# Kernel tuning notes

Hardware: AMD Instinct MI355X
Metric: run time of the kernel (lower is better)

The kernel has to match this reference:

```python
import jax, jax.numpy as jnp
import numpy as np

S_LEN, BATCH, HID, HEADS = 2048, 4, 1024, 16
HD = HID // HEADS


def setup_inputs() -> dict:
    key = jax.random.key(0)
    ks = jax.random.split(key, 6)

    def lin_w(k, out_dim, in_dim):
        return jax.random.normal(k, (out_dim, in_dim), jnp.float32) * (1.0 / np.sqrt(in_dim))

    return {
        "hidden_states": jax.random.normal(ks[0], (S_LEN, BATCH, HID), jnp.float32),
        "Wq": lin_w(ks[1], HID, HID), "bq": jnp.zeros((HID,), jnp.float32),
        "Wk": lin_w(ks[2], HID, HID), "bk": jnp.zeros((HID,), jnp.float32),
        "Wv": lin_w(ks[3], HID, HID), "bv": jnp.zeros((HID,), jnp.float32),
        "Wf": lin_w(ks[4], HEADS, HID), "bf": jnp.zeros((HEADS,), jnp.float32),
        "Wo": lin_w(ks[5], HID, HID), "bo": jnp.zeros((HID,), jnp.float32),
    }


def _forget_attention(hidden_states, Wq, bq, Wk, bk, Wv, bv, Wf, bf, Wo, bo):
    S, B, H = hidden_states.shape
    nh, hd = HEADS, HD

    def shape(x):
        return x.reshape(S, B, nh, hd)

    q = shape(hidden_states @ Wq.T + bq)
    k = shape(hidden_states @ Wk.T + bk)
    v = shape(hidden_states @ Wv.T + bv)

    # kernel_fn = elu(x) + 1
    phi_q = jax.nn.elu(q) + 1.0
    phi_k = jax.nn.elu(k) + 1.0

    f = jax.nn.sigmoid(hidden_states @ Wf.T + bf)  # [S, B, nh]

    # F_{t,j} = prod_{i=j+1}^{t} f_i  factorizes into the recurrence:
    #   S_t = f_t * S_{t-1} + phi_k_t (x) v_t ;  z_t = f_t * z_{t-1} + phi_k_t
    # out_t = (phi_q_t . S_t) / (phi_q_t . z_t + eps)
    def step(carry, xs):
        Sm, z = carry                      # [B,nh,hd,hd], [B,nh,hd]
        ft, pk, pq, vt = xs                # [B,nh], [B,nh,hd] x3
        fte = ft[..., None]
        Sm = fte[..., None] * Sm + pk[..., :, None] * vt[..., None, :]
        z = fte * z + pk
        num = jnp.einsum('bhd,bhde->bhe', pq, Sm)
        den = jnp.einsum('bhd,bhd->bh', pq, z)[..., None]
        return (Sm, z), num / (den + 1e-6)

    init = (jnp.zeros((B, nh, hd, hd), hidden_states.dtype),
            jnp.zeros((B, nh, hd), hidden_states.dtype))
    _, out = jax.lax.scan(step, init, (f, phi_k, phi_q, v))

    out = out.reshape(S, B, H) @ Wo.T + bo
    return out, f


def reference(hidden_states, Wq, bq, Wk, bk, Wv, bv, Wf, bf, Wo, bo):
    out, f = _forget_attention(hidden_states, Wq, bq, Wk, bk, Wv, bv, Wf, bf, Wo, bo)
    return (out, jnp.zeros_like(out), f)
```

## Files before the change

### kernel.cpp

```cpp
#include <hip/hip_runtime.h>
#include <hip/hip_bf16.h>
#include <math.h>

#define S_LEN 2048
#define BATCH 4
#define HID   1024
#define HEADS 16
#define HD    64
#define SB    (S_LEN*BATCH)
#define CHUNK 64
#define NCHUNK (S_LEN/CHUNK)
#define BH    (BATCH*HEADS)
#define NSTK  3200

typedef __bf16 bf16x8 __attribute__((ext_vector_type(8)));
typedef float  f32x4  __attribute__((ext_vector_type(4)));
typedef unsigned short ushort_t;
typedef unsigned short u16x8 __attribute__((ext_vector_type(8)));

__device__ __forceinline__ unsigned short f2bf(float x) {
    union { float f; unsigned int u; } un; un.f = x;
    unsigned int u = un.u;
    unsigned int r = (u + 0x7FFFu + ((u >> 16) & 1u)) >> 16;
    return (unsigned short)r;
}
__device__ __forceinline__ float bf2f(unsigned short s) {
    union { unsigned int u; float f; } un; un.u = ((unsigned int)s) << 16;
    return un.f;
}

#define NXU (SB*HID/4)
#define NW1 (NSTK*HID/4)
#define NW2 (HID*HID/4)
#define NBU (NSTK/4)
#define NTOT (NXU+NW1+NW2+NBU)

__global__ __launch_bounds__(256) void prep_kernel(
    const float* __restrict__ X,  const float* __restrict__ Wq,
    const float* __restrict__ Wk, const float* __restrict__ Wv,
    const float* __restrict__ Wf, const float* __restrict__ Wo,
    const float* __restrict__ bq, const float* __restrict__ bk,
    const float* __restrict__ bv, const float* __restrict__ bf,
    ushort_t* __restrict__ Xb, ushort_t* __restrict__ Wstk,
    ushort_t* __restrict__ Wob, float* __restrict__ bstk)
{
    const int i = blockIdx.x * 256 + threadIdx.x;
    if (i < NXU) {
        float4 v = ((const float4*)X)[i];
        ushort4 o; o.x=f2bf(v.x); o.y=f2bf(v.y); o.z=f2bf(v.z); o.w=f2bf(v.w);
        ((ushort4*)Xb)[i] = o;
    } else if (i < NXU + NW1) {
        const int idx4 = (i - NXU) * 4;
        const int row = idx4 >> 10, col = idx4 & 1023;
        float4 v;
        if      (row < 1024) v = *(const float4*)(Wq + (size_t)row*HID + col);
        else if (row < 2048) v = *(const float4*)(Wk + (size_t)(row-1024)*HID + col);
        else if (row < 3072) v = *(const float4*)(Wv + (size_t)(row-2048)*HID + col);
        else if (row < 3088) v = *(const float4*)(Wf + (size_t)(row-3072)*HID + col);
        else                 v = make_float4(0.f,0.f,0.f,0.f);
        ushort4 o; o.x=f2bf(v.x); o.y=f2bf(v.y); o.z=f2bf(v.z); o.w=f2bf(v.w);
        *(ushort4*)(Wstk + idx4) = o;
    } else if (i < NXU + NW1 + NW2) {
        const int idx4 = (i - NXU - NW1) * 4;
        float4 v = *(const float4*)(Wo + idx4);
        ushort4 o; o.x=f2bf(v.x); o.y=f2bf(v.y); o.z=f2bf(v.z); o.w=f2bf(v.w);
        *(ushort4*)(Wob + idx4) = o;
    } else if (i < NTOT) {
        const int idx4 = (i - NXU - NW1 - NW2) * 4;
        #pragma unroll
        for (int t = 0; t < 4; ++t) {
            const int c = idx4 + t;
            float v;
            if      (c < 1024) v = bq[c];
            else if (c < 2048) v = bk[c-1024];
            else if (c < 3072) v = bv[c-2048];
            else if (c < 3088) v = bf[c-3072];
            else               v = 0.f;
            bstk[c] = v;
        }
    }
}

__global__ __launch_bounds__(256) void qkvf_gemm(
    const ushort_t* __restrict__ X, const ushort_t* __restrict__ W,
    const float* __restrict__ bias,
    ushort_t* __restrict__ Q, ushort_t* __restrict__ Kr,
    ushort_t* __restrict__ V,
    float* __restrict__ f_out, float* __restrict__ logf_out)
{
    __shared__ ushort_t As[128 * 32];
    __shared__ ushort_t Bs[128 * 32];

    const int tid  = threadIdx.x;
    const int wave = tid >> 6, lane = tid & 63;
    const int waveM = wave >> 1, waveN = wave & 1;
    const int rowBase = blockIdx.x * 128;
    const int colBase = blockIdx.y * 128;
    const int K = HID;

    f32x4 acc[4][4];
    #pragma unroll
    for (int i = 0; i < 4; ++i)
        #pragma unroll
        for (int j = 0; j < 4; ++j)
            acc[i][j] = (f32x4){0.f, 0.f, 0.f, 0.f};

    const int srow = lane >> 2;
    const int scol = (lane & 3) * 8;

    const ushort_t* gA0 = X + (size_t)(rowBase + wave*16 + srow) * K + scol;
    const ushort_t* gB0 = W + (size_t)(colBase + wave*16 + srow) * K + scol;
    ushort_t* lA = As + (wave*16)*32;
    ushort_t* lB = Bs + (wave*16)*32;

    const int fr = lane & 15;
    const int fk = (lane >> 4) * 8;

    for (int k0 = 0; k0 < K; k0 += 32) {
        __builtin_amdgcn_global_load_lds(
            (const __attribute__((address_space(1))) void*)(gA0 + k0),
            (__attribute__((address_space(3))) void*)lA, 16, 0, 0);
        __builtin_amdgcn_global_load_lds(
            (const __attribute__((address_space(1))) void*)(gA0 + (size_t)64*K + k0),
            (__attribute__((address_space(3))) void*)(lA + 64*32), 16, 0, 0);
        __builtin_amdgcn_global_load_lds(
            (const __attribute__((address_space(1))) void*)(gB0 + k0),
            (__attribute__((address_space(3))) void*)lB, 16, 0, 0);
        __builtin_amdgcn_global_load_lds(
            (const __attribute__((address_space(1))) void*)(gB0 + (size_t)64*K + k0),
            (__attribute__((address_space(3))) void*)(lB + 64*32), 16, 0, 0);

        __syncthreads();

        bf16x8 a[4], b[4];
        #pragma unroll
        for (int i = 0; i < 4; ++i)
            a[i] = *(const bf16x8*)(As + (waveM*64 + i*16 + fr)*32 + fk);
        #pragma unroll
        for (int j = 0; j < 4; ++j)
            b[j] = *(const bf16x8*)(Bs + (waveN*64 + j*16 + fr)*32 + fk);

        #pragma unroll
        for (int i = 0; i < 4; ++i)
            #pragma unroll
            for (int j = 0; j < 4; ++j)
                acc[i][j] = __builtin_amdgcn_mfma_f32_16x16x32_bf16(
                    a[i], b[j], acc[i][j], 0, 0, 0);

        __syncthreads();
    }

    const int er = (lane >> 4) * 4;
    const int ec = lane & 15;
    #pragma unroll
    for (int i = 0; i < 4; ++i) {
        #pragma unroll
        for (int j = 0; j < 4; ++j) {
            const int r0 = rowBase + waveM*64 + i*16 + er;
            const int c0 = colBase + waveN*64 + j*16;
            if (c0 >= 3088) continue;
            const int c  = c0 + ec;
            const float bv = bias[c];
            #pragma unroll
            for (int k = 0; k < 4; ++k) {
                float v = acc[i][j][k] + bv;
                const int r = r0 + k;
                if (c0 < 1024) {
                    v = (v > 0.f) ? (v + 1.f) : __expf(v);
                    Q[(size_t)r * HID + c] = f2bf(v);
                } else if (c0 < 2048) {
                    v = (v > 0.f) ? (v + 1.f) : __expf(v);
                    Kr[(size_t)r * HID + (c - 1024)] = f2bf(v);
                } else if (c0 < 3072) {
                    V[(size_t)r * HID + (c - 2048)] = f2bf(v);
                } else {
                    const int n = c - 3072;
                    const float fv = 1.f / (1.f + __expf(-v));
                    f_out[(size_t)r * HEADS + n]    = fv;
                    logf_out[(size_t)r * HEADS + n] = -__logf(1.f + __expf(-v));
                }
            }
        }
    }
}

__global__ __launch_bounds__(256) void gemm_out(
    const ushort_t* __restrict__ X, const ushort_t* __restrict__ W,
    const float* __restrict__ bias, float* __restrict__ Y,
    float* __restrict__ Yzero)
{
    __shared__ ushort_t As[128 * 32];
    __shared__ ushort_t Bs[128 * 32];

    const int tid  = threadIdx.x;
    const int wave = tid >> 6, lane = tid & 63;
    const int waveM = wave >> 1, waveN = wave & 1;
    const int rowBase = blockIdx.x * 128;
    const int colBase = blockIdx.y * 128;
    const int K = HID, N = HID;

    f32x4 acc[4][4];
    #pragma unroll
    for (int i = 0; i < 4; ++i)
        #pragma unroll
        for (int j = 0; j < 4; ++j)
            acc[i][j] = (f32x4){0.f, 0.f, 0.f, 0.f};

    const int srow = lane >> 2;
    const int scol = (lane & 3) * 8;

    const ushort_t* gA0 = X + (size_t)(rowBase + wave*16 + srow) * K + scol;
    const ushort_t* gB0 = W + (size_t)(colBase + wave*16 + srow) * K + scol;
    ushort_t* lA = As + (wave*16)*32;
    ushort_t* lB = Bs + (wave*16)*32;

    const int fr = lane & 15;
    const int fk = (lane >> 4) * 8;

    for (int k0 = 0; k0 < K; k0 += 32) {
        __builtin_amdgcn_global_load_lds(
            (const __attribute__((address_space(1))) void*)(gA0 + k0),
            (__attribute__((address_space(3))) void*)lA, 16, 0, 0);
        __builtin_amdgcn_global_load_lds(
            (const __attribute__((address_space(1))) void*)(gA0 + (size_t)64*K + k0),
            (__attribute__((address_space(3))) void*)(lA + 64*32), 16, 0, 0);
        __builtin_amdgcn_global_load_lds(
            (const __attribute__((address_space(1))) void*)(gB0 + k0),
            (__attribute__((address_space(3))) void*)lB, 16, 0, 0);
        __builtin_amdgcn_global_load_lds(
            (const __attribute__((address_space(1))) void*)(gB0 + (size_t)64*K + k0),
            (__attribute__((address_space(3))) void*)(lB + 64*32), 16, 0, 0);

        __syncthreads();

        bf16x8 a[4], b[4];
        #pragma unroll
        for (int i = 0; i < 4; ++i)
            a[i] = *(const bf16x8*)(As + (waveM*64 + i*16 + fr)*32 + fk);
        #pragma unroll
        for (int j = 0; j < 4; ++j)
            b[j] = *(const bf16x8*)(Bs + (waveN*64 + j*16 + fr)*32 + fk);

        #pragma unroll
        for (int i = 0; i < 4; ++i)
            #pragma unroll
            for (int j = 0; j < 4; ++j)
                acc[i][j] = __builtin_amdgcn_mfma_f32_16x16x32_bf16(
                    a[i], b[j], acc[i][j], 0, 0, 0);

        __syncthreads();
    }

    const int er = (lane >> 4) * 4;
    const int ec = lane & 15;
    #pragma unroll
    for (int i = 0; i < 4; ++i) {
        #pragma unroll
        for (int j = 0; j < 4; ++j) {
            const int r0 = rowBase + waveM*64 + i*16 + er;
            const int c  = colBase + waveN*64 + j*16 + ec;
            const float bv = bias[c];
            #pragma unroll
            for (int k = 0; k < 4; ++k) {
                const size_t off = (size_t)(r0 + k) * N + c;
                Y[off] = acc[i][j][k] + bv;
                Yzero[off] = 0.f;
            }
        }
    }
}

__global__ __launch_bounds__(256) void pass1_kernel(
    const ushort_t* __restrict__ Kp, const ushort_t* __restrict__ Vp,
    const float* __restrict__ logf,
    ushort_t* __restrict__ Schunk, float* __restrict__ zchunk,
    float* __restrict__ Dchunk)
{
    __shared__ __align__(16) char smem[18688];
    ushort_t* vsT = (ushort_t*)smem;
    ushort_t* kTd = (ushort_t*)(smem + 9216);
    float*    exd = (float*)(smem + 18432);

    const int chunk = blockIdx.x;
    const int bh = blockIdx.y;
    const int b = bh >> 4, h = bh & 15;
    const int tid = threadIdx.x;
    const int wv = tid >> 6, ln = tid & 63;
    const int fr = ln & 15, q4 = ln >> 4;
    const size_t slot = (size_t)bh * NCHUNK + chunk;

    u16x8 vreg[2], kreg[2];
    #pragma unroll
    for (int it = 0; it < 2; ++it) {
        const int u = it*256 + tid;
        const int j = u >> 3, d8 = (u & 7) * 8;
        const size_t base = (size_t)((chunk*64 + j)*BATCH + b)*HID + h*HD + d8;
        vreg[it] = *(const u16x8*)(Vp + base);
        kreg[it] = *(const u16x8*)(Kp + base);
    }
    if (tid < 64) {
        float v = logf[(size_t)((chunk*64 + tid)*BATCH + b) * HEADS + h];
        #pragma unroll
        for (int off = 1; off < 64; off <<= 1) {
            float n = __shfl_up(v, off);
            if (tid >= off) v += n;
        }
        const float tot = __shfl(v, 63);
        exd[tid] = __expf(tot - v);
        if (tid == 63) Dchunk[slot] = __expf(tot);
    }
    __syncthreads();

    #pragma unroll
    for (int it = 0; it < 2; ++it) {
        const int u = it*256 + tid;
        const int j = u >> 3, d8 = (u & 7) * 8;
        const float ex = exd[j];
        #pragma unroll
        for (int i = 0; i < 8; ++i) {
            vsT[(d8+i)*72 + j] = vreg[it][i];
            kTd[(d8+i)*72 + j] = f2bf(bf2f(kreg[it][i]) * ex);
        }
    }
    __syncthreads();

    f32x4 acc[4];
    #pragma unroll
    for (int nt = 0; nt < 4; ++nt) acc[nt] = (f32x4){0.f,0.f,0.f,0.f};
    #pragma unroll
    for (int k0 = 0; k0 < 64; k0 += 32) {
        bf16x8 av = *(const bf16x8*)(vsT + (wv*16 + fr)*72 + k0 + q4*8);
        #pragma unroll
        for (int nt = 0; nt < 4; ++nt) {
            bf16x8 bk = *(const bf16x8*)(kTd + (nt*16 + fr)*72 + k0 + q4*8);
            acc[nt] = __builtin_amdgcn_mfma_f32_16x16x32_bf16(av, bk, acc[nt], 0, 0, 0);
        }
    }

    if (wv == 0) {
        u16x8 onesu;
        #pragma unroll
        for (int i = 0; i < 8; ++i) onesu[i] = 0x3F80;
        const bf16x8 ones = *(const bf16x8*)&onesu;
        f32x4 zacc[4];
        #pragma unroll
        for (int nt = 0; nt < 4; ++nt) zacc[nt] = (f32x4){0.f,0.f,0.f,0.f};
        #pragma unroll
        for (int k0 = 0; k0 < 64; k0 += 32) {
            #pragma unroll
            for (int nt = 0; nt < 4; ++nt) {
                bf16x8 bk = *(const bf16x8*)(kTd + (nt*16 + fr)*72 + k0 + q4*8);
                zacc[nt] = __builtin_amdgcn_mfma_f32_16x16x32_bf16(ones, bk, zacc[nt], 0, 0, 0);
            }
        }
        if (q4 == 0) {
            #pragma unroll
            for (int nt = 0; nt < 4; ++nt)
                zchunk[slot*64 + nt*16 + fr] = zacc[nt][0];
        }
    }

    ushort_t* sp = Schunk + slot * 4096;
    #pragma unroll
    for (int nt = 0; nt < 4; ++nt) {
        #pragma unroll
        for (int r = 0; r < 4; ++r) {
            const int e = wv*16 + q4*4 + r;
            sp[e*64 + nt*16 + fr] = f2bf(acc[nt][r]);
        }
    }
}

__global__ __launch_bounds__(256) void pass2_kernel(
    ushort_t* __restrict__ Schunk, float* __restrict__ zchunk,
    const float* __restrict__ Dchunk)
{
    const int bh = blockIdx.x;
    const int tid = threadIdx.x;

    float Sprev[16];
    #pragma unroll
    for (int i = 0; i < 16; ++i) Sprev[i] = 0.f;
    float zprev = 0.f;

    const size_t base  = (size_t)bh * NCHUNK * 4096;
    const size_t zbase = (size_t)bh * NCHUNK * 64;

    ushort_t b0[16], b1[16];
    float z0v = 0.f, z1v = 0.f;
    #pragma unroll
    for (int i = 0; i < 16; ++i) {
        b0[i] = Schunk[base + 0*4096 + i*256 + tid];
        b1[i] = Schunk[base + 1*4096 + i*256 + tid];
    }
    if (tid < 64) {
        z0v = zchunk[zbase + 0*64 + tid];
        z1v = zchunk[zbase + 1*64 + tid];
    }

    for (int c = 0; c < NCHUNK; ++c) {
        const float D = Dchunk[bh * NCHUNK + c];
        ushort_t* sp = Schunk + base + (size_t)c * 4096;
        #pragma unroll
        for (int i = 0; i < 16; ++i) {
            const float contrib = bf2f(b0[i]);
            sp[i*256 + tid] = f2bf(Sprev[i]);
            Sprev[i] = D * Sprev[i] + contrib;
            b0[i] = b1[i];
        }
        if (tid < 64) {
            const float zc = z0v;
            zchunk[zbase + (size_t)c * 64 + tid] = zprev;
            zprev = D * zprev + zc;
            z0v = z1v;
        }
        if (c + 2 < NCHUNK) {
            #pragma unroll
            for (int i = 0; i < 16; ++i)
                b1[i] = Schunk[base + (size_t)(c+2)*4096 + i*256 + tid];
            if (tid < 64) z1v = zchunk[zbase + (size_t)(c+2)*64 + tid];
        }
    }
}

__global__ __launch_bounds__(256) void pass3_kernel(
    const ushort_t* __restrict__ Qp, const ushort_t* __restrict__ Kp,
    const ushort_t* __restrict__ Vp, const float* __restrict__ logf,
    const ushort_t* __restrict__ S0, const float* __restrict__ z0,
    ushort_t* __restrict__ AO)
{
    __shared__ __align__(16) char smem[28928];
    ushort_t* qs  = (ushort_t*)smem;
    ushort_t* ks  = (ushort_t*)(smem + 9216);
    ushort_t* vsT = (ushort_t*)(smem + 9216);
    ushort_t* psA = (ushort_t*)(smem + 18432);
    float* cc  = (float*)(smem + 27648);
    float* exT = (float*)(smem + 27904);
    float* qz  = (float*)(smem + 28160);
    float* den = (float*)(smem + 28416);
    float* zz  = (float*)(smem + 28672);

    const int chunk = blockIdx.x;
    const int bh = blockIdx.y;
    const int b = bh >> 4, h = bh & 15;
    const int tid = threadIdx.x;
    const int wv = tid >> 6, ln = tid & 63;
    const int fr = ln & 15, q4 = ln >> 4;
    const size_t slot = (size_t)bh * NCHUNK + chunk;

    u16x8 vreg[2];
    #pragma unroll
    for (int it = 0; it < 2; ++it) {
        const int u = it*256 + tid;
        const int j = u >> 3, d8 = (u & 7) * 8;
        vreg[it] = *(const u16x8*)(Vp + (size_t)((chunk*64 + j)*BATCH + b)*HID + h*HD + d8);
    }

    if (tid < 64) {
        zz[tid] = z0[slot * 64 + tid];
        float v = logf[(size_t)((chunk*64 + tid)*BATCH + b) * HEADS + h];
        #pragma unroll
        for (int off = 1; off < 64; off <<= 1) {
            float n = __shfl_up(v, off);
            if (tid >= off) v += n;
        }
        cc[tid]  = v;
        exT[tid] = __expf(v);
    }
    #pragma unroll
    for (int it = 0; it < 2; ++it) {
        const int u = it*256 + tid;
        const int r = u >> 3, c8 = (u & 7) * 8;
        const size_t goff = (size_t)((chunk*64 + r)*BATCH + b) * HID + h*HD + c8;
        *(u16x8*)(qs + r*72 + c8) = *(const u16x8*)(Qp + goff);
        *(u16x8*)(ks + r*72 + c8) = *(const u16x8*)(Kp + goff);
    }
    __syncthreads();

    f32x4 pacc[4];
    #pragma unroll
    for (int nt = 0; nt < 4; ++nt) pacc[nt] = (f32x4){0.f,0.f,0.f,0.f};
    #pragma unroll
    for (int k0 = 0; k0 < 64; k0 += 32) {
        bf16x8 af = *(const bf16x8*)(qs + (wv*16 + fr)*72 + k0 + q4*8);
        #pragma unroll
        for (int nt = 0; nt < 4; ++nt) {
            bf16x8 bfr = *(const bf16x8*)(ks + (nt*16 + fr)*72 + k0 + q4*8);
            pacc[nt] = __builtin_amdgcn_mfma_f32_16x16x32_bf16(af, bfr, pacc[nt], 0, 0, 0);
        }
    }
    {
        const int t = wv*16 + fr;
        const int d0 = q4 * 16;
        float s = 0.f;
        #pragma unroll
        for (int i = 0; i < 16; ++i)
            s += bf2f(qs[t*72 + d0 + i]) * zz[d0 + i];
        s += __shfl_xor(s, 16);
        s += __shfl_xor(s, 32);
        if (q4 == 0) qz[t] = s;
    }
    __syncthreads();

    #pragma unroll
    for (int it = 0; it < 2; ++it) {
        const int u = it*256 + tid;
        const int j = u >> 3, d8 = (u & 7) * 8;
        #pragma unroll
        for (int i = 0; i < 8; ++i)
            vsT[(d8+i)*72 + j] = vreg[it][i];
    }
    {
        float rs[4] = {0.f, 0.f, 0.f, 0.f};
        float cct[4];
        #pragma unroll
        for (int r = 0; r < 4; ++r) cct[r] = cc[wv*16 + q4*4 + r];
        #pragma unroll
        for (int nt = 0; nt < 4; ++nt) {
            const int j = nt*16 + fr;
            const float ccj = cc[j];
            #pragma unroll
            for (int r = 0; r < 4; ++r) {
                const int t = wv*16 + q4*4 + r;
                float p = (j <= t) ? pacc[nt][r] * __expf(cct[r] - ccj) : 0.f;
                rs[r] += p;
                psA[t*72 + j] = f2bf(p);
            }
        }
        #pragma unroll
        for (int m = 1; m < 16; m <<= 1) {
            #pragma unroll
            for (int r = 0; r < 4; ++r) rs[r] += __shfl_xor(rs[r], m);
        }
        if (fr == 0) {
            #pragma unroll
            for (int r = 0; r < 4; ++r) {
                const int t = wv*16 + q4*4 + r;
                den[t] = rs[r] + exT[t] * qz[t] + 1e-6f;
            }
        }
    }
    __syncthreads();

    f32x4 oacc[4], oacc2[4];
    #pragma unroll
    for (int nt = 0; nt < 4; ++nt) {
        oacc[nt]  = (f32x4){0.f,0.f,0.f,0.f};
        oacc2[nt] = (f32x4){0.f,0.f,0.f,0.f};
    }
    const ushort_t* S0p = S0 + slot * 4096;
    #pragma unroll
    for (int k0 = 0; k0 < 64; k0 += 32) {
        const int k8 = k0 + q4*8;
        bf16x8 ap = *(const bf16x8*)(psA + (wv*16 + fr)*72 + k8);
        bf16x8 aq = *(const bf16x8*)(qs  + (wv*16 + fr)*72 + k8);
        #pragma unroll
        for (int nt = 0; nt < 4; ++nt) {
            bf16x8 bv = *(const bf16x8*)(vsT + (nt*16 + fr)*72 + k8);
            oacc[nt] = __builtin_amdgcn_mfma_f32_16x16x32_bf16(ap, bv, oacc[nt], 0, 0, 0);
            bf16x8 sb = *(const bf16x8*)(S0p + (nt*16 + fr)*64 + k8);
            oacc2[nt] = __builtin_amdgcn_mfma_f32_16x16x32_bf16(aq, sb, oacc2[nt], 0, 0, 0);
        }
    }
    #pragma unroll
    for (int nt = 0; nt < 4; ++nt) {
        const int e = nt*16 + fr;
        #pragma unroll
        for (int r = 0; r < 4; ++r) {
            const int t = wv*16 + q4*4 + r;
            const float v = (oacc[nt][r] + exT[t] * oacc2[nt][r]) / den[t];
            AO[(size_t)((chunk*64 + t)*BATCH + b) * HID + h*HD + e] = f2bf(v);
        }
    }
}

extern "C" void kernel_launch(void* const* d_in, const int* in_sizes, int n_in,
                              void* d_out, int out_size, void* d_ws, size_t ws_size,
                              hipStream_t stream) {
    const float* X  = (const float*)d_in[0];
    const float* Wq = (const float*)d_in[1];
    const float* bq = (const float*)d_in[2];
    const float* Wk = (const float*)d_in[3];
    const float* bk = (const float*)d_in[4];
    const float* Wv = (const float*)d_in[5];
    const float* bv = (const float*)d_in[6];
    const float* Wf = (const float*)d_in[7];
    const float* bf = (const float*)d_in[8];
    const float* Wo = (const float*)d_in[9];
    const float* bo = (const float*)d_in[10];

    float* out = (float*)d_out;
    const size_t OUT_SLOT = (size_t)SB * HID;

    char* ws = (char*)d_ws;
    ushort_t* wsXb   = (ushort_t*)ws;
    ushort_t* wsWstk = wsXb + (size_t)SB * HID;
    ushort_t* wsWob  = wsWstk + (size_t)NSTK * HID;
    ushort_t* wsQ    = wsWob + (size_t)HID * HID;
    ushort_t* wsK    = wsQ + (size_t)SB * HID;
    ushort_t* wsV    = wsK + (size_t)SB * HID;
    float* wsBstk = (float*)(wsV + (size_t)SB * HID);
    float* wsLogf = wsBstk + NSTK;
    ushort_t* wsS  = (ushort_t*)(wsLogf + (size_t)SB * HEADS);
    float* wsZ    = (float*)(wsS + (size_t)BH * NCHUNK * HD * HD);
    float* wsD    = wsZ + (size_t)BH * NCHUNK * HD;

    prep_kernel<<<(NTOT + 255)/256, 256, 0, stream>>>(
        X, Wq, Wk, Wv, Wf, Wo, bq, bk, bv, bf,
        wsXb, wsWstk, wsWob, wsBstk);

    dim3 qgrid(SB/128, NSTK/128);
    qkvf_gemm<<<qgrid, 256, 0, stream>>>(
        wsXb, wsWstk, wsBstk, wsQ, wsK, wsV,
        out + 2*OUT_SLOT, wsLogf);

    dim3 sgrid(NCHUNK, BH);
    pass1_kernel<<<sgrid, 256, 0, stream>>>(wsK, wsV, wsLogf, wsS, wsZ, wsD);
    pass2_kernel<<<BH, 256, 0, stream>>>(wsS, wsZ, wsD);
    pass3_kernel<<<sgrid, 256, 0, stream>>>(wsQ, wsK, wsV, wsLogf, wsS, wsZ, wsXb);

    dim3 ogrid(SB/128, HID/128);
    gemm_out<<<ogrid, 256, 0, stream>>>(wsXb, wsWob, bo, out, out + OUT_SLOT);
}
```

Baseline: 290.5 us.

## Double-buffer LDS in both GEMMs, memset zero output, cache chunk decays in LDS

```diff
diff --git a/kernel.cpp b/kernel.cpp
--- a/kernel.cpp
+++ b/kernel.cpp
@@ -28,6 +28,10 @@
     union { unsigned int u; float f; } un; un.u = ((unsigned int)s) << 16;
     return un.f;
 }
+
+#define GLL16(src, dst) __builtin_amdgcn_global_load_lds( \
+    (const __attribute__((address_space(1))) void*)(src), \
+    (__attribute__((address_space(3))) void*)(dst), 16, 0, 0)
 
 #define NXU (SB*HID/4)
 #define NW1 (NSTK*HID/4)
@@ -88,8 +92,8 @@
     ushort_t* __restrict__ V,
     float* __restrict__ f_out, float* __restrict__ logf_out)
 {
-    __shared__ ushort_t As[128 * 32];
-    __shared__ ushort_t Bs[128 * 32];
+    __shared__ ushort_t As[2][128 * 32];
+    __shared__ ushort_t Bs[2][128 * 32];
 
     const int tid  = threadIdx.x;
     const int wave = tid >> 6, lane = tid & 63;
@@ -110,35 +114,41 @@
 
     const ushort_t* gA0 = X + (size_t)(rowBase + wave*16 + srow) * K + scol;
     const ushort_t* gB0 = W + (size_t)(colBase + wave*16 + srow) * K + scol;
-    ushort_t* lA = As + (wave*16)*32;
-    ushort_t* lB = Bs + (wave*16)*32;
+    const int ldsWaveOff = (wave*16)*32;
 
     const int fr = lane & 15;
     const int fk = (lane >> 4) * 8;
 
+    {
+        ushort_t* lA = As[0] + ldsWaveOff;
+        ushort_t* lB = Bs[0] + ldsWaveOff;
+        GLL16(gA0,                  lA);
+        GLL16(gA0 + (size_t)64*K,   lA + 64*32);
+        GLL16(gB0,                  lB);
+        GLL16(gB0 + (size_t)64*K,   lB + 64*32);
+    }
+    __syncthreads();
+
+    int cur = 0;
+    #pragma unroll 2
     for (int k0 = 0; k0 < K; k0 += 32) {
-        __builtin_amdgcn_global_load_lds(
-            (const __attribute__((address_space(1))) void*)(gA0 + k0),
-            (__attribute__((address_space(3))) void*)lA, 16, 0, 0);
-        __builtin_amdgcn_global_load_lds(
-            (const __attribute__((address_space(1))) void*)(gA0 + (size_t)64*K + k0),
-            (__attribute__((address_space(3))) void*)(lA + 64*32), 16, 0, 0);
-        __builtin_amdgcn_global_load_lds(
-            (const __attribute__((address_space(1))) void*)(gB0 + k0),
-            (__attribute__((address_space(3))) void*)lB, 16, 0, 0);
-        __builtin_amdgcn_global_load_lds(
-            (const __attribute__((address_space(1))) void*)(gB0 + (size_t)64*K + k0),
-            (__attribute__((address_space(3))) void*)(lB + 64*32), 16, 0, 0);
-
-        __syncthreads();
+        if (k0 + 32 < K) {
+            const int nxt = cur ^ 1;
+            ushort_t* lA = As[nxt] + ldsWaveOff;
+            ushort_t* lB = Bs[nxt] + ldsWaveOff;
+            GLL16(gA0 + k0 + 32,                lA);
+            GLL16(gA0 + (size_t)64*K + k0 + 32, lA + 64*32);
+            GLL16(gB0 + k0 + 32,                lB);
+            GLL16(gB0 + (size_t)64*K + k0 + 32, lB + 64*32);
+        }
 
         bf16x8 a[4], b[4];
         #pragma unroll
         for (int i = 0; i < 4; ++i)
-            a[i] = *(const bf16x8*)(As + (waveM*64 + i*16 + fr)*32 + fk);
+            a[i] = *(const bf16x8*)(As[cur] + (waveM*64 + i*16 + fr)*32 + fk);
         #pragma unroll
         for (int j = 0; j < 4; ++j)
-            b[j] = *(const bf16x8*)(Bs + (waveN*64 + j*16 + fr)*32 + fk);
+            b[j] = *(const bf16x8*)(Bs[cur] + (waveN*64 + j*16 + fr)*32 + fk);
 
         #pragma unroll
         for (int i = 0; i < 4; ++i)
@@ -148,6 +158,7 @@
                     a[i], b[j], acc[i][j], 0, 0, 0);
 
         __syncthreads();
+        cur ^= 1;
     }
 
     const int er = (lane >> 4) * 4;
@@ -186,11 +197,10 @@
 
 __global__ __launch_bounds__(256) void gemm_out(
     const ushort_t* __restrict__ X, const ushort_t* __restrict__ W,
-    const float* __restrict__ bias, float* __restrict__ Y,
-    float* __restrict__ Yzero)
+    const float* __restrict__ bias, float* __restrict__ Y)
 {
-    __shared__ ushort_t As[128 * 32];
-    __shared__ ushort_t Bs[128 * 32];
+    __shared__ ushort_t As[2][128 * 32];
+    __shared__ ushort_t Bs[2][128 * 32];
 
     const int tid  = threadIdx.x;
     const int wave = tid >> 6, lane = tid & 63;
@@ -211,35 +221,41 @@
 
     const ushort_t* gA0 = X + (size_t)(rowBase + wave*16 + srow) * K + scol;
     const ushort_t* gB0 = W + (size_t)(colBase + wave*16 + srow) * K + scol;
-    ushort_t* lA = As + (wave*16)*32;
-    ushort_t* lB = Bs + (wave*16)*32;
+    const int ldsWaveOff = (wave*16)*32;
 
     const int fr = lane & 15;
     const int fk = (lane >> 4) * 8;
 
+    {
+        ushort_t* lA = As[0] + ldsWaveOff;
+        ushort_t* lB = Bs[0] + ldsWaveOff;
+        GLL16(gA0,                  lA);
+        GLL16(gA0 + (size_t)64*K,   lA + 64*32);
+        GLL16(gB0,                  lB);
+        GLL16(gB0 + (size_t)64*K,   lB + 64*32);
+    }
+    __syncthreads();
+
+    int cur = 0;
+    #pragma unroll 2
     for (int k0 = 0; k0 < K; k0 += 32) {
-        __builtin_amdgcn_global_load_lds(
-            (const __attribute__((address_space(1))) void*)(gA0 + k0),
-            (__attribute__((address_space(3))) void*)lA, 16, 0, 0);
-        __builtin_amdgcn_global_load_lds(
-            (const __attribute__((address_space(1))) void*)(gA0 + (size_t)64*K + k0),
-            (__attribute__((address_space(3))) void*)(lA + 64*32), 16, 0, 0);
-        __builtin_amdgcn_global_load_lds(
-            (const __attribute__((address_space(1))) void*)(gB0 + k0),
-            (__attribute__((address_space(3))) void*)lB, 16, 0, 0);
-        __builtin_amdgcn_global_load_lds(
-            (const __attribute__((address_space(1))) void*)(gB0 + (size_t)64*K + k0),
-            (__attribute__((address_space(3))) void*)(lB + 64*32), 16, 0, 0);
-
-        __syncthreads();
+        if (k0 + 32 < K) {
+            const int nxt = cur ^ 1;
+            ushort_t* lA = As[nxt] + ldsWaveOff;
+            ushort_t* lB = Bs[nxt] + ldsWaveOff;
+            GLL16(gA0 + k0 + 32,                lA);
+            GLL16(gA0 + (size_t)64*K + k0 + 32, lA + 64*32);
+            GLL16(gB0 + k0 + 32,                lB);
+            GLL16(gB0 + (size_t)64*K + k0 + 32, lB + 64*32);
+        }
 
         bf16x8 a[4], b[4];
         #pragma unroll
         for (int i = 0; i < 4; ++i)
-            a[i] = *(const bf16x8*)(As + (waveM*64 + i*16 + fr)*32 + fk);
+            a[i] = *(const bf16x8*)(As[cur] + (waveM*64 + i*16 + fr)*32 + fk);
         #pragma unroll
         for (int j = 0; j < 4; ++j)
-            b[j] = *(const bf16x8*)(Bs + (waveN*64 + j*16 + fr)*32 + fk);
+            b[j] = *(const bf16x8*)(Bs[cur] + (waveN*64 + j*16 + fr)*32 + fk);
 
         #pragma unroll
         for (int i = 0; i < 4; ++i)
@@ -249,6 +265,7 @@
                     a[i], b[j], acc[i][j], 0, 0, 0);
 
         __syncthreads();
+        cur ^= 1;
     }
 
     const int er = (lane >> 4) * 4;
@@ -264,7 +281,6 @@
             for (int k = 0; k < 4; ++k) {
                 const size_t off = (size_t)(r0 + k) * N + c;
                 Y[off] = acc[i][j][k] + bv;
-                Yzero[off] = 0.f;
             }
         }
     }
@@ -375,8 +391,11 @@
     ushort_t* __restrict__ Schunk, float* __restrict__ zchunk,
     const float* __restrict__ Dchunk)
 {
+    __shared__ float Ds[NCHUNK];
     const int bh = blockIdx.x;
     const int tid = threadIdx.x;
+
+    if (tid < NCHUNK) Ds[tid] = Dchunk[bh * NCHUNK + tid];
 
     float Sprev[16];
     #pragma unroll
@@ -397,9 +416,10 @@
         z0v = zchunk[zbase + 0*64 + tid];
         z1v = zchunk[zbase + 1*64 + tid];
     }
+    __syncthreads();
 
     for (int c = 0; c < NCHUNK; ++c) {
-        const float D = Dchunk[bh * NCHUNK + c];
+        const float D = Ds[c];
         ushort_t* sp = Schunk + base + (size_t)c * 4096;
         #pragma unroll
         for (int i = 0; i < 16; ++i) {
@@ -605,6 +625,8 @@
     float* wsZ    = (float*)(wsS + (size_t)BH * NCHUNK * HD * HD);
     float* wsD    = wsZ + (size_t)BH * NCHUNK * HD;
 
+    hipMemsetAsync(out + OUT_SLOT, 0, OUT_SLOT * sizeof(float), stream);
+
     prep_kernel<<<(NTOT + 255)/256, 256, 0, stream>>>(
         X, Wq, Wk, Wv, Wf, Wo, bq, bk, bv, bf,
         wsXb, wsWstk, wsWob, wsBstk);
@@ -620,5 +642,5 @@
     pass3_kernel<<<sgrid, 256, 0, stream>>>(wsQ, wsK, wsV, wsLogf, wsS, wsZ, wsXb);
 
     dim3 ogrid(SB/128, HID/128);
-    gemm_out<<<ogrid, 256, 0, stream>>>(wsXb, wsWob, bo, out, out + OUT_SLOT);
-}
+    gemm_out<<<ogrid, 256, 0, stream>>>(wsXb, wsWob, bo, out);
+}
```

New measurement: 303.1 us. 1.04x slower.

## Rewrite QKVF GEMM with 256x256 tiles and triple-buffered async LDS pipeline

Applied to the files above, without the earlier changes.

```diff
diff --git a/kernel.cpp b/kernel.cpp
--- a/kernel.cpp
+++ b/kernel.cpp
@@ -11,7 +11,7 @@
 #define CHUNK 64
 #define NCHUNK (S_LEN/CHUNK)
 #define BH    (BATCH*HEADS)
-#define NSTK  3200
+#define NSTK  3328
 
 typedef __bf16 bf16x8 __attribute__((ext_vector_type(8)));
 typedef float  f32x4  __attribute__((ext_vector_type(4)));
@@ -28,6 +28,12 @@
     union { unsigned int u; float f; } un; un.u = ((unsigned int)s) << 16;
     return un.f;
 }
+
+#define GLL16(src, dst) __builtin_amdgcn_global_load_lds( \
+    (const __attribute__((address_space(1))) void*)(src), \
+    (__attribute__((address_space(3))) void*)(dst), 16, 0, 0)
+
+#define BAR()  asm volatile("s_barrier" ::: "memory")
 
 #define NXU (SB*HID/4)
 #define NW1 (NSTK*HID/4)
@@ -81,83 +87,121 @@
     }
 }
 
-__global__ __launch_bounds__(256) void qkvf_gemm(
+#define QTILES 32
+#define QBLOCKS 416
+
+__global__ __launch_bounds__(512, 2) void qkvf_gemm256(
     const ushort_t* __restrict__ X, const ushort_t* __restrict__ W,
     const float* __restrict__ bias,
     ushort_t* __restrict__ Q, ushort_t* __restrict__ Kr,
     ushort_t* __restrict__ V,
     float* __restrict__ f_out, float* __restrict__ logf_out)
 {
-    __shared__ ushort_t As[128 * 32];
-    __shared__ ushort_t Bs[128 * 32];
+    __shared__ ushort_t lds[3 * 16384];
 
     const int tid  = threadIdx.x;
     const int wave = tid >> 6, lane = tid & 63;
-    const int waveM = wave >> 1, waveN = wave & 1;
-    const int rowBase = blockIdx.x * 128;
-    const int colBase = blockIdx.y * 128;
+    const int wm = wave >> 2, wn = wave & 3;
+    const int fr = lane & 15, q4 = lane >> 4;
     const int K = HID;
 
-    f32x4 acc[4][4];
-    #pragma unroll
-    for (int i = 0; i < 4; ++i)
+    const int wg = ((blockIdx.x & 7) * 52) + (blockIdx.x >> 3);
+    const int rowBase = (wg & 31) << 8;
+    const int colBase = (wg >> 5) << 8;
+
+    const int sRow = lane >> 2;
+    const int sCol = (((lane & 3) ^ ((lane >> 3) & 3)) << 3);
+    const ushort_t* gA0 = X + (size_t)(rowBase + wave*32 + sRow) * K + sCol;
+    const ushort_t* gB0 = W + (size_t)(colBase + wave*32 + sRow) * K + sCol;
+    const int stA = wave * 1024;
+    const int stB = 8192 + wave * 1024;
+
+    const int sl = ((q4 ^ ((fr >> 1) & 3)) << 3);
+    const int aBase = wm*4096 + fr*32 + sl;
+    const int bBase = 8192 + wn*2048 + fr*32 + sl;
+
+    f32x4 acc[8][4];
+    #pragma unroll
+    for (int i = 0; i < 8; ++i)
         #pragma unroll
         for (int j = 0; j < 4; ++j)
             acc[i][j] = (f32x4){0.f, 0.f, 0.f, 0.f};
 
-    const int srow = lane >> 2;
-    const int scol = (lane & 3) * 8;
-
-    const ushort_t* gA0 = X + (size_t)(rowBase + wave*16 + srow) * K + scol;
-    const ushort_t* gB0 = W + (size_t)(colBase + wave*16 + srow) * K + scol;
-    ushort_t* lA = As + (wave*16)*32;
-    ushort_t* lB = Bs + (wave*16)*32;
-
-    const int fr = lane & 15;
-    const int fk = (lane >> 4) * 8;
-
-    for (int k0 = 0; k0 < K; k0 += 32) {
-        __builtin_amdgcn_global_load_lds(
-            (const __attribute__((address_space(1))) void*)(gA0 + k0),
-            (__attribute__((address_space(3))) void*)lA, 16, 0, 0);
-        __builtin_amdgcn_global_load_lds(
-            (const __attribute__((address_space(1))) void*)(gA0 + (size_t)64*K + k0),
-            (__attribute__((address_space(3))) void*)(lA + 64*32), 16, 0, 0);
-        __builtin_amdgcn_global_load_lds(
-            (const __attribute__((address_space(1))) void*)(gB0 + k0),
-            (__attribute__((address_space(3))) void*)lB, 16, 0, 0);
-        __builtin_amdgcn_global_load_lds(
-            (const __attribute__((address_space(1))) void*)(gB0 + (size_t)64*K + k0),
-            (__attribute__((address_space(3))) void*)(lB + 64*32), 16, 0, 0);
-
-        __syncthreads();
-
-        bf16x8 a[4], b[4];
+    GLL16(gA0,                     lds + stA);
+    GLL16(gA0 + (size_t)16*K,      lds + stA + 512);
+    GLL16(gB0,                     lds + stB);
+    GLL16(gB0 + (size_t)16*K,      lds + stB + 512);
+    GLL16(gA0 + 32,                lds + 16384 + stA);
+    GLL16(gA0 + (size_t)16*K + 32, lds + 16384 + stA + 512);
+    GLL16(gB0 + 32,                lds + 16384 + stB);
+    GLL16(gB0 + (size_t)16*K + 32, lds + 16384 + stB + 512);
+    asm volatile("s_waitcnt vmcnt(4)" ::: "memory");
+    BAR();
+
+    int bi = 0, si = 2;
+    const ushort_t* gAs = gA0 + 64;
+    const ushort_t* gBs = gB0 + 64;
+
+    for (int t = 0; t < QTILES; ++t) {
+        const ushort_t* Lb = lds + bi * 16384;
+        ushort_t* Ls = lds + si * 16384;
+
+        bf16x8 af[4], bfr[4];
         #pragma unroll
         for (int i = 0; i < 4; ++i)
-            a[i] = *(const bf16x8*)(As + (waveM*64 + i*16 + fr)*32 + fk);
+            af[i] = *(const bf16x8*)(Lb + aBase + i*512);
         #pragma unroll
         for (int j = 0; j < 4; ++j)
-            b[j] = *(const bf16x8*)(Bs + (waveN*64 + j*16 + fr)*32 + fk);
-
+            bfr[j] = *(const bf16x8*)(Lb + bBase + j*512);
+        if (t < QTILES - 2) {
+            GLL16(gAs,                Ls + stA);
+            GLL16(gAs + (size_t)16*K, Ls + stA + 512);
+        }
+        BAR();
+        __builtin_amdgcn_s_setprio(1);
         #pragma unroll
         for (int i = 0; i < 4; ++i)
             #pragma unroll
             for (int j = 0; j < 4; ++j)
                 acc[i][j] = __builtin_amdgcn_mfma_f32_16x16x32_bf16(
-                    a[i], b[j], acc[i][j], 0, 0, 0);
-
-        __syncthreads();
-    }
-
-    const int er = (lane >> 4) * 4;
-    const int ec = lane & 15;
-    #pragma unroll
-    for (int i = 0; i < 4; ++i) {
+                    af[i], bfr[j], acc[i][j], 0, 0, 0);
+        __builtin_amdgcn_s_setprio(0);
+        BAR();
+
+        bf16x8 ag[4];
+        #pragma unroll
+        for (int i = 0; i < 4; ++i)
+            ag[i] = *(const bf16x8*)(Lb + aBase + 2048 + i*512);
+        if (t < QTILES - 2) {
+            GLL16(gBs,                Ls + stB);
+            GLL16(gBs + (size_t)16*K, Ls + stB + 512);
+        }
+        BAR();
+        __builtin_amdgcn_s_setprio(1);
+        #pragma unroll
+        for (int i = 0; i < 4; ++i)
+            #pragma unroll
+            for (int j = 0; j < 4; ++j)
+                acc[4+i][j] = __builtin_amdgcn_mfma_f32_16x16x32_bf16(
+                    ag[i], bfr[j], acc[4+i][j], 0, 0, 0);
+        __builtin_amdgcn_s_setprio(0);
+        if (t < QTILES - 2)       { asm volatile("s_waitcnt vmcnt(4)" ::: "memory"); }
+        else if (t == QTILES - 2) { asm volatile("s_waitcnt vmcnt(0)" ::: "memory"); }
+        BAR();
+
+        bi = (bi == 2) ? 0 : bi + 1;
+        si = (si == 2) ? 0 : si + 1;
+        gAs += 32; gBs += 32;
+    }
+
+    const int er = q4 * 4;
+    const int ec = fr;
+    #pragma unroll
+    for (int i = 0; i < 8; ++i) {
         #pragma unroll
         for (int j = 0; j < 4; ++j) {
-            const int r0 = rowBase + waveM*64 + i*16 + er;
-            const int c0 = colBase + waveN*64 + j*16;
+            const int r0 = rowBase + wm*128 + i*16 + er;
+            const int c0 = colBase + wn*64 + j*16;
             if (c0 >= 3088) continue;
             const int c  = c0 + ec;
             const float bv = bias[c];
@@ -186,8 +230,7 @@
 
 __global__ __launch_bounds__(256) void gemm_out(
     const ushort_t* __restrict__ X, const ushort_t* __restrict__ W,
-    const float* __restrict__ bias, float* __restrict__ Y,
-    float* __restrict__ Yzero)
+    const float* __restrict__ bias, float* __restrict__ Y)
 {
     __shared__ ushort_t As[128 * 32];
     __shared__ ushort_t Bs[128 * 32];
@@ -218,18 +261,10 @@
     const int fk = (lane >> 4) * 8;
 
     for (int k0 = 0; k0 < K; k0 += 32) {
-        __builtin_amdgcn_global_load_lds(
-            (const __attribute__((address_space(1))) void*)(gA0 + k0),
-            (__attribute__((address_space(3))) void*)lA, 16, 0, 0);
-        __builtin_amdgcn_global_load_lds(
-            (const __attribute__((address_space(1))) void*)(gA0 + (size_t)64*K + k0),
-            (__attribute__((address_space(3))) void*)(lA + 64*32), 16, 0, 0);
-        __builtin_amdgcn_global_load_lds(
-            (const __attribute__((address_space(1))) void*)(gB0 + k0),
-            (__attribute__((address_space(3))) void*)lB, 16, 0, 0);
-        __builtin_amdgcn_global_load_lds(
-            (const __attribute__((address_space(1))) void*)(gB0 + (size_t)64*K + k0),
-            (__attribute__((address_space(3))) void*)(lB + 64*32), 16, 0, 0);
+        GLL16(gA0 + k0,                lA);
+        GLL16(gA0 + (size_t)64*K + k0, lA + 64*32);
+        GLL16(gB0 + k0,                lB);
+        GLL16(gB0 + (size_t)64*K + k0, lB + 64*32);
 
         __syncthreads();
 
@@ -264,7 +299,6 @@
             for (int k = 0; k < 4; ++k) {
                 const size_t off = (size_t)(r0 + k) * N + c;
                 Y[off] = acc[i][j][k] + bv;
-                Yzero[off] = 0.f;
             }
         }
     }
@@ -375,8 +409,11 @@
     ushort_t* __restrict__ Schunk, float* __restrict__ zchunk,
     const float* __restrict__ Dchunk)
 {
+    __shared__ float Ds[NCHUNK];
     const int bh = blockIdx.x;
     const int tid = threadIdx.x;
+
+    if (tid < NCHUNK) Ds[tid] = Dchunk[bh * NCHUNK + tid];
 
     float Sprev[16];
     #pragma unroll
@@ -397,9 +434,10 @@
         z0v = zchunk[zbase + 0*64 + tid];
         z1v = zchunk[zbase + 1*64 + tid];
     }
+    __syncthreads();
 
     for (int c = 0; c < NCHUNK; ++c) {
-        const float D = Dchunk[bh * NCHUNK + c];
+        const float D = Ds[c];
         ushort_t* sp = Schunk + base + (size_t)c * 4096;
         #pragma unroll
         for (int i = 0; i < 16; ++i) {
@@ -605,12 +643,13 @@
     float* wsZ    = (float*)(wsS + (size_t)BH * NCHUNK * HD * HD);
     float* wsD    = wsZ + (size_t)BH * NCHUNK * HD;
 
+    hipMemsetAsync(out + OUT_SLOT, 0, OUT_SLOT * sizeof(float), stream);
+
     prep_kernel<<<(NTOT + 255)/256, 256, 0, stream>>>(
         X, Wq, Wk, Wv, Wf, Wo, bq, bk, bv, bf,
         wsXb, wsWstk, wsWob, wsBstk);
 
-    dim3 qgrid(SB/128, NSTK/128);
-    qkvf_gemm<<<qgrid, 256, 0, stream>>>(
+    qkvf_gemm256<<<QBLOCKS, 512, 0, stream>>>(
         wsXb, wsWstk, wsBstk, wsQ, wsK, wsV,
         out + 2*OUT_SLOT, wsLogf);
 
@@ -620,5 +659,5 @@
     pass3_kernel<<<sgrid, 256, 0, stream>>>(wsQ, wsK, wsV, wsLogf, wsS, wsZ, wsXb);
 
     dim3 ogrid(SB/128, HID/128);
-    gemm_out<<<ogrid, 256, 0, stream>>>(wsXb, wsWob, bo, out, out + OUT_SLOT);
-}
+    gemm_out<<<ogrid, 256, 0, stream>>>(wsXb, wsWob, bo, out);
+}
```

Result: slower. 362.3 us (+24.8%).

## Split chunk-state scan across 8 blocks per head and memset zero output

Applied to the files above, without the earlier changes.

```diff
diff --git a/kernel.cpp b/kernel.cpp
--- a/kernel.cpp
+++ b/kernel.cpp
@@ -28,6 +28,10 @@
     union { unsigned int u; float f; } un; un.u = ((unsigned int)s) << 16;
     return un.f;
 }
+
+#define GLL16(src, dst) __builtin_amdgcn_global_load_lds( \
+    (const __attribute__((address_space(1))) void*)(src), \
+    (__attribute__((address_space(3))) void*)(dst), 16, 0, 0)
 
 #define NXU (SB*HID/4)
 #define NW1 (NSTK*HID/4)
@@ -117,18 +121,10 @@
     const int fk = (lane >> 4) * 8;
 
     for (int k0 = 0; k0 < K; k0 += 32) {
-        __builtin_amdgcn_global_load_lds(
-            (const __attribute__((address_space(1))) void*)(gA0 + k0),
-            (__attribute__((address_space(3))) void*)lA, 16, 0, 0);
-        __builtin_amdgcn_global_load_lds(
-            (const __attribute__((address_space(1))) void*)(gA0 + (size_t)64*K + k0),
-            (__attribute__((address_space(3))) void*)(lA + 64*32), 16, 0, 0);
-        __builtin_amdgcn_global_load_lds(
-            (const __attribute__((address_space(1))) void*)(gB0 + k0),
-            (__attribute__((address_space(3))) void*)lB, 16, 0, 0);
-        __builtin_amdgcn_global_load_lds(
-            (const __attribute__((address_space(1))) void*)(gB0 + (size_t)64*K + k0),
-            (__attribute__((address_space(3))) void*)(lB + 64*32), 16, 0, 0);
+        GLL16(gA0 + k0,                lA);
+        GLL16(gA0 + (size_t)64*K + k0, lA + 64*32);
+        GLL16(gB0 + k0,                lB);
+        GLL16(gB0 + (size_t)64*K + k0, lB + 64*32);
 
         __syncthreads();
 
@@ -186,8 +182,7 @@
 
 __global__ __launch_bounds__(256) void gemm_out(
     const ushort_t* __restrict__ X, const ushort_t* __restrict__ W,
-    const float* __restrict__ bias, float* __restrict__ Y,
-    float* __restrict__ Yzero)
+    const float* __restrict__ bias, float* __restrict__ Y)
 {
     __shared__ ushort_t As[128 * 32];
     __shared__ ushort_t Bs[128 * 32];
@@ -218,18 +213,10 @@
     const int fk = (lane >> 4) * 8;
 
     for (int k0 = 0; k0 < K; k0 += 32) {
-        __builtin_amdgcn_global_load_lds(
-            (const __attribute__((address_space(1))) void*)(gA0 + k0),
-            (__attribute__((address_space(3))) void*)lA, 16, 0, 0);
-        __builtin_amdgcn_global_load_lds(
-            (const __attribute__((address_space(1))) void*)(gA0 + (size_t)64*K + k0),
-            (__attribute__((address_space(3))) void*)(lA + 64*32), 16, 0, 0);
-        __builtin_amdgcn_global_load_lds(
-            (const __attribute__((address_space(1))) void*)(gB0 + k0),
-            (__attribute__((address_space(3))) void*)lB, 16, 0, 0);
-        __builtin_amdgcn_global_load_lds(
-            (const __attribute__((address_space(1))) void*)(gB0 + (size_t)64*K + k0),
-            (__attribute__((address_space(3))) void*)(lB + 64*32), 16, 0, 0);
+        GLL16(gA0 + k0,                lA);
+        GLL16(gA0 + (size_t)64*K + k0, lA + 64*32);
+        GLL16(gB0 + k0,                lB);
+        GLL16(gB0 + (size_t)64*K + k0, lB + 64*32);
 
         __syncthreads();
 
@@ -264,7 +251,6 @@
             for (int k = 0; k < 4; ++k) {
                 const size_t off = (size_t)(r0 + k) * N + c;
                 Y[off] = acc[i][j][k] + bv;
-                Yzero[off] = 0.f;
             }
         }
     }
@@ -375,40 +361,44 @@
     ushort_t* __restrict__ Schunk, float* __restrict__ zchunk,
     const float* __restrict__ Dchunk)
 {
-    const int bh = blockIdx.x;
+    __shared__ float Ds[NCHUNK];
+    const int bh  = blockIdx.x >> 3;
+    const int sl  = blockIdx.x & 7;
     const int tid = threadIdx.x;
 
-    float Sprev[16];
-    #pragma unroll
-    for (int i = 0; i < 16; ++i) Sprev[i] = 0.f;
+    if (tid < NCHUNK) Ds[tid] = Dchunk[bh * NCHUNK + tid];
+
+    float Sprev[2] = {0.f, 0.f};
     float zprev = 0.f;
 
-    const size_t base  = (size_t)bh * NCHUNK * 4096;
+    const size_t base  = (size_t)bh * NCHUNK * 4096 + sl * 512;
     const size_t zbase = (size_t)bh * NCHUNK * 64;
-
-    ushort_t b0[16], b1[16];
+    const bool doZ = (sl == 0) && (tid < 64);
+
+    ushort_t b0[2], b1[2];
     float z0v = 0.f, z1v = 0.f;
     #pragma unroll
-    for (int i = 0; i < 16; ++i) {
+    for (int i = 0; i < 2; ++i) {
         b0[i] = Schunk[base + 0*4096 + i*256 + tid];
         b1[i] = Schunk[base + 1*4096 + i*256 + tid];
     }
-    if (tid < 64) {
+    if (doZ) {
         z0v = zchunk[zbase + 0*64 + tid];
         z1v = zchunk[zbase + 1*64 + tid];
     }
+    __syncthreads();
 
     for (int c = 0; c < NCHUNK; ++c) {
-        const float D = Dchunk[bh * NCHUNK + c];
+        const float D = Ds[c];
         ushort_t* sp = Schunk + base + (size_t)c * 4096;
         #pragma unroll
-        for (int i = 0; i < 16; ++i) {
+        for (int i = 0; i < 2; ++i) {
             const float contrib = bf2f(b0[i]);
             sp[i*256 + tid] = f2bf(Sprev[i]);
             Sprev[i] = D * Sprev[i] + contrib;
             b0[i] = b1[i];
         }
-        if (tid < 64) {
+        if (doZ) {
             const float zc = z0v;
             zchunk[zbase + (size_t)c * 64 + tid] = zprev;
             zprev = D * zprev + zc;
@@ -416,9 +406,9 @@
         }
         if (c + 2 < NCHUNK) {
             #pragma unroll
-            for (int i = 0; i < 16; ++i)
+            for (int i = 0; i < 2; ++i)
                 b1[i] = Schunk[base + (size_t)(c+2)*4096 + i*256 + tid];
-            if (tid < 64) z1v = zchunk[zbase + (size_t)(c+2)*64 + tid];
+            if (doZ) z1v = zchunk[zbase + (size_t)(c+2)*64 + tid];
         }
     }
 }
@@ -605,6 +595,8 @@
     float* wsZ    = (float*)(wsS + (size_t)BH * NCHUNK * HD * HD);
     float* wsD    = wsZ + (size_t)BH * NCHUNK * HD;
 
+    hipMemsetAsync(out + OUT_SLOT, 0, OUT_SLOT * sizeof(float), stream);
+
     prep_kernel<<<(NTOT + 255)/256, 256, 0, stream>>>(
         X, Wq, Wk, Wv, Wf, Wo, bq, bk, bv, bf,
         wsXb, wsWstk, wsWob, wsBstk);
@@ -616,9 +608,9 @@
 
     dim3 sgrid(NCHUNK, BH);
     pass1_kernel<<<sgrid, 256, 0, stream>>>(wsK, wsV, wsLogf, wsS, wsZ, wsD);
-    pass2_kernel<<<BH, 256, 0, stream>>>(wsS, wsZ, wsD);
+    pass2_kernel<<<BH*8, 256, 0, stream>>>(wsS, wsZ, wsD);
     pass3_kernel<<<sgrid, 256, 0, stream>>>(wsQ, wsK, wsV, wsLogf, wsS, wsZ, wsXb);
 
     dim3 ogrid(SB/128, HID/128);
-    gemm_out<<<ogrid, 256, 0, stream>>>(wsXb, wsWob, bo, out, out + OUT_SLOT);
-}
+    gemm_out<<<ogrid, 256, 0, stream>>>(wsXb, wsWob, bo, out);
+}
```

Result: no change. 285.9 us (-1.6%).
